# Kernel tuning notes

Hardware: AMD Instinct MI355X
Metric: run time of the kernel (lower is better)

The kernel has to match this reference:

```python
import jax, jax.numpy as jnp
import numpy as np

BLOCK = 64  # block_size from config
NEG_INF = -1e9


def setup_inputs() -> dict:
    key = jax.random.key(0)
    k1, k2, k3, k4 = jax.random.split(key, 4)
    B, H, S, D = 2, 8, 2048, 64
    nb = S // BLOCK  # 32 blocks per side
    query = jax.random.normal(k1, (B, H, S, D), dtype=jnp.float32)
    key_t = jax.random.normal(k2, (B, H, S, D), dtype=jnp.float32)
    value = jax.random.normal(k3, (B, H, S, D), dtype=jnp.float32)
    # binary block mask; force diagonal blocks on so every row has >=1 valid key
    mat = jax.random.randint(k4, (nb, nb), 0, 2).astype(jnp.int32)
    mat = mat.at[jnp.arange(nb), jnp.arange(nb)].set(1)
    mask = jnp.ones((B, S), dtype=jnp.float32)  # padding mask (1 = keep)
    return {"query": query, "key": key_t, "value": value, "mask": mask, "mat": mat}


def reference(query, key, value, mask, mat):
    # Upsample block mask [nb, nb] -> dense [S, S] (nearest, like nn.Upsample)
    block_dense = jnp.repeat(jnp.repeat(mat, BLOCK, axis=0), BLOCK, axis=1) > 0
    # Block-sparse QK^T: only positions inside nonzero blocks participate.
    scores = jnp.einsum('bhqd,bhkd->bhqk', query, key)
    # Additive padding-mask bias, as in the original: 1e6 * (1 - mask)
    scores = scores - 1e6 * (1.0 - mask)[:, None, None, :]
    # Positions outside the block pattern are excluded from the softmax.
    scores = jnp.where(block_dense[None, None, :, :], scores, NEG_INF)
    attn = jax.nn.softmax(scores, axis=-1)
    out = jnp.einsum('bhqk,bhkd->bhqd', attn, value)
    return out
```

## Files before the change

kernel.cpp:

```cpp
#include <hip/hip_runtime.h>


typedef __attribute__((ext_vector_type(8))) short short8;
typedef __attribute__((ext_vector_type(4))) short short4_;
typedef __attribute__((ext_vector_type(4))) float float4_;

#define B_   2
#define H_   8
#define S_   2048
#define D_   64
#define NB_  32
#define KP   72

__device__ __forceinline__ short f2bf(float f) {
    union { float f; unsigned int u; } x; x.f = f;
    unsigned int r = x.u + 0x7FFFu + ((x.u >> 16) & 1u);
    return (short)(r >> 16);
}
__device__ __forceinline__ float bf2f(short s) {
    union { unsigned int u; float f; } x; x.u = ((unsigned int)(unsigned short)s) << 16;
    return x.f;
}

__global__ __launch_bounds__(256)
void preconvert_kernel(const float* __restrict__ K, const float* __restrict__ V,
                       short* __restrict__ Khi, short* __restrict__ Klo,
                       short* __restrict__ Vtb) {
    __shared__ short vn[64 * KP];
    const int tid = threadIdx.x;
    const int kt  = blockIdx.x;
    const int bh  = blockIdx.y;
    const size_t tb = ((size_t)bh * S_ + kt * 64) * D_;

#pragma unroll
    for (int it = 0; it < 4; ++it) {
        int i = tid + it * 256;
        int row = i >> 4, c4 = (i & 15) * 4;
        float4_ kv = *(const float4_*)(K + tb + row * D_ + c4);
        short4_ hi, lo;
#pragma unroll
        for (int e = 0; e < 4; ++e) {
            hi[e] = f2bf(kv[e]);
            lo[e] = f2bf(kv[e] - bf2f(hi[e]));
        }
        *(short4_*)(Khi + tb + row * D_ + c4) = hi;
        *(short4_*)(Klo + tb + row * D_ + c4) = lo;
        float4_ vv = *(const float4_*)(V + tb + row * D_ + c4);
        short4_ vb;
#pragma unroll
        for (int e = 0; e < 4; ++e) vb[e] = f2bf(vv[e]);
        *(short4_*)&vn[row * KP + c4] = vb;
    }
    __syncthreads();
#pragma unroll
    for (int it = 0; it < 2; ++it) {
        int i = tid + it * 256;
        int rowd = i >> 3, key8 = (i & 7) * 8;
        short8 o;
#pragma unroll
        for (int e = 0; e < 8; ++e) o[e] = vn[(key8 + e) * KP + rowd];
        *(short8*)(Vtb + (((size_t)(bh * NB_ + kt)) * 64 + rowd) * 64 + key8) = o;
    }
}

__global__ __launch_bounds__(256, 2)
void attn_mfma_pl(const float* __restrict__ Q,
                  const float* __restrict__ Msk,
                  const int* __restrict__ Mat,
                  float* __restrict__ O,
                  const short* __restrict__ Khi_g,
                  const short* __restrict__ Klo_g,
                  const short* __restrict__ Vtb_g) {
    __shared__ __align__(16) short lds[4 * 64 * KP];
    short* Khi = lds;
    short* Klo = lds + 64 * KP;
    short* Vt  = lds + 2 * 64 * KP;
    short* Pl  = lds + 3 * 64 * KP;

    const int tid  = threadIdx.x;
    const int wave = tid >> 6;
    const int lane = tid & 63;
    const int c    = lane & 15;
    const int quad = lane >> 4;

    const int qb = blockIdx.x;
    const int bh = blockIdx.y;
    const int b  = bh / H_;
    const size_t base = (size_t)bh * S_ * D_;

    const int row0 = tid >> 3,          col0 = (tid & 7) * 8;
    const int row1 = (tid + 256) >> 3,  col1 = (tid & 7) * 8;

    short8 qh0, qh1, ql0, ql1;
    {
        const float* qp = Q + base + (size_t)(qb * 64 + wave * 16 + c) * D_ + quad * 8;
#pragma unroll
        for (int e = 0; e < 8; ++e) {
            float f0 = qp[e], f1 = qp[e + 32];
            qh0[e] = f2bf(f0); ql0[e] = f2bf(f0 - bf2f(qh0[e]));
            qh1[e] = f2bf(f1); ql1[e] = f2bf(f1 - bf2f(qh1[e]));
        }
    }

    float4_ o[4];
    float l_part[4];
#pragma unroll
    for (int t = 0; t < 4; ++t) { o[t][0] = 0.f; o[t][1] = 0.f; o[t][2] = 0.f; o[t][3] = 0.f; }
#pragma unroll
    for (int j = 0; j < 4; ++j) l_part[j] = 0.f;

    unsigned long long bm = __ballot(Mat[qb * NB_ + (lane & 31)] != 0);
    unsigned int mbits = (unsigned int)(bm & 0xFFFFFFFFull);

    short8 sK0, sK1, sL0, sL1, sV0, sV1;
    float  biasn[4];

    int kb = __builtin_ctz(mbits);
    mbits &= mbits - 1;
    {
        const short* kh = Khi_g + base + (size_t)kb * 64 * D_;
        const short* kl = Klo_g + base + (size_t)kb * 64 * D_;
        const short* vt = Vtb_g + ((size_t)(bh * NB_ + kb)) * 64 * 64;
        sK0 = *(const short8*)(kh + row0 * 64 + col0);
        sK1 = *(const short8*)(kh + row1 * 64 + col1);
        sL0 = *(const short8*)(kl + row0 * 64 + col0);
        sL1 = *(const short8*)(kl + row1 * 64 + col1);
        sV0 = *(const short8*)(vt + row0 * 64 + col0);
        sV1 = *(const short8*)(vt + row1 * 64 + col1);
#pragma unroll
        for (int t = 0; t < 4; ++t)
            biasn[t] = -1.0e6f * (1.0f - Msk[(size_t)b * S_ + kb * 64 + t * 16 + c]);
    }

    for (;;) {
        __syncthreads();
        *(short8*)&Khi[row0 * KP + col0] = sK0;
        *(short8*)&Khi[row1 * KP + col1] = sK1;
        *(short8*)&Klo[row0 * KP + col0] = sL0;
        *(short8*)&Klo[row1 * KP + col1] = sL1;
        *(short8*)&Vt[row0 * KP + col0]  = sV0;
        *(short8*)&Vt[row1 * KP + col1]  = sV1;
        float biasc[4];
#pragma unroll
        for (int t = 0; t < 4; ++t) biasc[t] = biasn[t];
        __syncthreads();

        const bool have_next = (mbits != 0);
        if (have_next) {
            kb = __builtin_ctz(mbits);
            mbits &= mbits - 1;
            const short* kh = Khi_g + base + (size_t)kb * 64 * D_;
            const short* kl = Klo_g + base + (size_t)kb * 64 * D_;
            const short* vt = Vtb_g + ((size_t)(bh * NB_ + kb)) * 64 * 64;
            sK0 = *(const short8*)(kh + row0 * 64 + col0);
            sK1 = *(const short8*)(kh + row1 * 64 + col1);
            sL0 = *(const short8*)(kl + row0 * 64 + col0);
            sL1 = *(const short8*)(kl + row1 * 64 + col1);
            sV0 = *(const short8*)(vt + row0 * 64 + col0);
            sV1 = *(const short8*)(vt + row1 * 64 + col1);
#pragma unroll
            for (int t = 0; t < 4; ++t)
                biasn[t] = -1.0e6f * (1.0f - Msk[(size_t)b * S_ + kb * 64 + t * 16 + c]);
        }

        float4_ sc[4];
#pragma unroll
        for (int t = 0; t < 4; ++t) { sc[t][0] = 0.f; sc[t][1] = 0.f; sc[t][2] = 0.f; sc[t][3] = 0.f; }
#pragma unroll
        for (int t = 0; t < 4; ++t) {
            const short* kph = &Khi[(t * 16 + c) * KP + quad * 8];
            const short* kpl = &Klo[(t * 16 + c) * KP + quad * 8];
            short8 kh0 = *(const short8*)(kph);
            short8 kh1 = *(const short8*)(kph + 32);
            short8 kl0 = *(const short8*)(kpl);
            short8 kl1 = *(const short8*)(kpl + 32);
            sc[t] = __builtin_amdgcn_mfma_f32_16x16x32_bf16(qh0, kh0, sc[t], 0, 0, 0);
            sc[t] = __builtin_amdgcn_mfma_f32_16x16x32_bf16(qh1, kh1, sc[t], 0, 0, 0);
            sc[t] = __builtin_amdgcn_mfma_f32_16x16x32_bf16(qh0, kl0, sc[t], 0, 0, 0);
            sc[t] = __builtin_amdgcn_mfma_f32_16x16x32_bf16(qh1, kl1, sc[t], 0, 0, 0);
            sc[t] = __builtin_amdgcn_mfma_f32_16x16x32_bf16(ql0, kh0, sc[t], 0, 0, 0);
            sc[t] = __builtin_amdgcn_mfma_f32_16x16x32_bf16(ql1, kh1, sc[t], 0, 0, 0);
        }

        short* Pw = Pl + wave * 16 * KP;
#pragma unroll
        for (int t = 0; t < 4; ++t) {
#pragma unroll
            for (int j = 0; j < 4; ++j) {
                float p = __expf(sc[t][j] + biasc[t]);
                l_part[j] += p;
                Pw[(quad * 4 + j) * KP + t * 16 + c] = f2bf(p);
            }
        }

        const short* pp = Pl + wave * 16 * KP + c * KP + quad * 8;
        short8 pa0 = *(const short8*)(pp);
        short8 pa1 = *(const short8*)(pp + 32);

#pragma unroll
        for (int t = 0; t < 4; ++t) {
            const short* vp = &Vt[(t * 16 + c) * KP + quad * 8];
            short8 vb0 = *(const short8*)(vp);
            short8 vb1 = *(const short8*)(vp + 32);
            o[t] = __builtin_amdgcn_mfma_f32_16x16x32_bf16(pa0, vb0, o[t], 0, 0, 0);
            o[t] = __builtin_amdgcn_mfma_f32_16x16x32_bf16(pa1, vb1, o[t], 0, 0, 0);
        }

        if (!have_next) break;
    }

#pragma unroll
    for (int j = 0; j < 4; ++j) {
        float rs = l_part[j];
        rs += __shfl_xor(rs, 1);
        rs += __shfl_xor(rs, 2);
        rs += __shfl_xor(rs, 4);
        rs += __shfl_xor(rs, 8);
        float inv = 1.0f / rs;
        size_t rowoff = base + (size_t)(qb * 64 + wave * 16 + quad * 4 + j) * D_;
#pragma unroll
        for (int t = 0; t < 4; ++t)
            O[rowoff + t * 16 + c] = o[t][j] * inv;
    }
}

__global__ __launch_bounds__(256, 2)
void attn_mfma_fb(const float* __restrict__ Q,
                  const float* __restrict__ K,
                  const float* __restrict__ V,
                  const float* __restrict__ Msk,
                  const int* __restrict__ Mat,
                  float* __restrict__ O) {
    __shared__ __align__(16) short lds[4 * 64 * KP];
    short* Khi = lds;
    short* Klo = lds + 64 * KP;
    short* Vt  = lds + 2 * 64 * KP;
    short* Pl  = lds + 3 * 64 * KP;

    const int tid  = threadIdx.x;
    const int wave = tid >> 6;
    const int lane = tid & 63;
    const int c    = lane & 15;
    const int quad = lane >> 4;

    const int qb = blockIdx.x;
    const int bh = blockIdx.y;
    const int b  = bh / H_;
    const size_t base = (size_t)bh * S_ * D_;

    short8 qh0, qh1, ql0, ql1;
    {
        const float* qp = Q + base + (size_t)(qb * 64 + wave * 16 + c) * D_ + quad * 8;
#pragma unroll
        for (int e = 0; e < 8; ++e) {
            float f0 = qp[e], f1 = qp[e + 32];
            qh0[e] = f2bf(f0); ql0[e] = f2bf(f0 - bf2f(qh0[e]));
            qh1[e] = f2bf(f1); ql1[e] = f2bf(f1 - bf2f(qh1[e]));
        }
    }

    float4_ o[4];
    float l_part[4];
#pragma unroll
    for (int t = 0; t < 4; ++t) { o[t][0] = 0.f; o[t][1] = 0.f; o[t][2] = 0.f; o[t][3] = 0.f; }
#pragma unroll
    for (int j = 0; j < 4; ++j) l_part[j] = 0.f;

    for (int kb = 0; kb < NB_; ++kb) {
        if (Mat[qb * NB_ + kb] == 0) continue;

        __syncthreads();
        {
            const float* kg = K + base + (size_t)kb * 64 * D_;
            const float* vg = V + base + (size_t)kb * 64 * D_;
#pragma unroll
            for (int it = 0; it < 4; ++it) {
                int i = tid + it * 256;
                int row = i >> 4, c4 = (i & 15) * 4;
                float4_ kv = *(const float4_*)(kg + row * D_ + c4);
                short4_ hi, lo;
#pragma unroll
                for (int e = 0; e < 4; ++e) {
                    hi[e] = f2bf(kv[e]);
                    lo[e] = f2bf(kv[e] - bf2f(hi[e]));
                }
                *(short4_*)&Khi[row * KP + c4] = hi;
                *(short4_*)&Klo[row * KP + c4] = lo;
                float4_ vv = *(const float4_*)(vg + row * D_ + c4);
#pragma unroll
                for (int e = 0; e < 4; ++e) Vt[(c4 + e) * KP + row] = f2bf(vv[e]);
            }
        }
        __syncthreads();

        float4_ sc[4];
#pragma unroll
        for (int t = 0; t < 4; ++t) { sc[t][0] = 0.f; sc[t][1] = 0.f; sc[t][2] = 0.f; sc[t][3] = 0.f; }
#pragma unroll
        for (int t = 0; t < 4; ++t) {
            const short* kph = &Khi[(t * 16 + c) * KP + quad * 8];
            const short* kpl = &Klo[(t * 16 + c) * KP + quad * 8];
            short8 kh0 = *(const short8*)(kph);
            short8 kh1 = *(const short8*)(kph + 32);
            short8 kl0 = *(const short8*)(kpl);
            short8 kl1 = *(const short8*)(kpl + 32);
            sc[t] = __builtin_amdgcn_mfma_f32_16x16x32_bf16(qh0, kh0, sc[t], 0, 0, 0);
            sc[t] = __builtin_amdgcn_mfma_f32_16x16x32_bf16(qh1, kh1, sc[t], 0, 0, 0);
            sc[t] = __builtin_amdgcn_mfma_f32_16x16x32_bf16(qh0, kl0, sc[t], 0, 0, 0);
            sc[t] = __builtin_amdgcn_mfma_f32_16x16x32_bf16(qh1, kl1, sc[t], 0, 0, 0);
            sc[t] = __builtin_amdgcn_mfma_f32_16x16x32_bf16(ql0, kh0, sc[t], 0, 0, 0);
            sc[t] = __builtin_amdgcn_mfma_f32_16x16x32_bf16(ql1, kh1, sc[t], 0, 0, 0);
        }

        short* Pw = Pl + wave * 16 * KP;
#pragma unroll
        for (int t = 0; t < 4; ++t) {
            float bias = -1.0e6f * (1.0f - Msk[(size_t)b * S_ + kb * 64 + t * 16 + c]);
#pragma unroll
            for (int j = 0; j < 4; ++j) {
                float p = __expf(sc[t][j] + bias);
                l_part[j] += p;
                Pw[(quad * 4 + j) * KP + t * 16 + c] = f2bf(p);
            }
        }

        const short* pp = Pl + wave * 16 * KP + c * KP + quad * 8;
        short8 pa0 = *(const short8*)(pp);
        short8 pa1 = *(const short8*)(pp + 32);

#pragma unroll
        for (int t = 0; t < 4; ++t) {
            const short* vp = &Vt[(t * 16 + c) * KP + quad * 8];
            short8 vb0 = *(const short8*)(vp);
            short8 vb1 = *(const short8*)(vp + 32);
            o[t] = __builtin_amdgcn_mfma_f32_16x16x32_bf16(pa0, vb0, o[t], 0, 0, 0);
            o[t] = __builtin_amdgcn_mfma_f32_16x16x32_bf16(pa1, vb1, o[t], 0, 0, 0);
        }
    }

#pragma unroll
    for (int j = 0; j < 4; ++j) {
        float rs = l_part[j];
        rs += __shfl_xor(rs, 1);
        rs += __shfl_xor(rs, 2);
        rs += __shfl_xor(rs, 4);
        rs += __shfl_xor(rs, 8);
        float inv = 1.0f / rs;
        size_t rowoff = base + (size_t)(qb * 64 + wave * 16 + quad * 4 + j) * D_;
#pragma unroll
        for (int t = 0; t < 4; ++t)
            O[rowoff + t * 16 + c] = o[t][j] * inv;
    }
}

extern "C" void kernel_launch(void* const* d_in, const int* in_sizes, int n_in,
                              void* d_out, int out_size, void* d_ws, size_t ws_size,
                              hipStream_t stream) {
    const float* q   = (const float*)d_in[0];
    const float* k   = (const float*)d_in[1];
    const float* v   = (const float*)d_in[2];
    const float* msk = (const float*)d_in[3];
    const int*   mat = (const int*)d_in[4];
    float*       out = (float*)d_out;

    const size_t elems = (size_t)B_ * H_ * S_ * D_;
    const size_t need  = 3 * elems * sizeof(short);
    const int use_pre  = (ws_size >= need) ? 1 : 0;

    short* khi = (short*)d_ws;
    short* klo = khi + elems;
    short* vtb = klo + elems;

    dim3 grid(NB_, B_ * H_);
    if (use_pre) {
        preconvert_kernel<<<grid, dim3(256), 0, stream>>>(k, v, khi, klo, vtb);
        attn_mfma_pl<<<grid, dim3(256), 0, stream>>>(q, msk, mat, out, khi, klo, vtb);
    } else {
        attn_mfma_fb<<<grid, dim3(256), 0, stream>>>(q, k, v, msk, mat, out);
    }
}
```

Baseline: 119.4 us.

## Replace split-bf16 QK^T with single fp16 MFMA and halve query tile

K is now preconverted to a single fp16 copy, and Q is converted to fp16 in-kernel. QK^T then uses two fp16 MFMAs per tile instead of six split hi/lo bf16 MFMAs, and the Klo workspace buffer and its loads are gone. The attention kernel also moves to 128-thread blocks covering 32 query rows, which doubles the grid. That gives more parallelism, but each K/V block is now staged twice as often across workgroups. The trade-off is lower precision in the scores: there is no max-subtraction before exp, so fp16 rounding of large logits could push results past tolerance.

Result: faster. 112.9 us (-5.4%).

```diff
diff --git a/kernel.cpp b/kernel.cpp
--- a/kernel.cpp
+++ b/kernel.cpp
@@ -4,6 +4,7 @@
 typedef __attribute__((ext_vector_type(8))) short short8;
 typedef __attribute__((ext_vector_type(4))) short short4_;
 typedef __attribute__((ext_vector_type(4))) float float4_;
+typedef __attribute__((ext_vector_type(8))) _Float16 half8_;
 
 #define B_   2
 #define H_   8
@@ -21,11 +22,14 @@
     union { unsigned int u; float f; } x; x.u = ((unsigned int)(unsigned short)s) << 16;
     return x.f;
 }
+__device__ __forceinline__ short f2h(float f) {
+    _Float16 h = (_Float16)f;
+    return __builtin_bit_cast(short, h);
+}
 
 __global__ __launch_bounds__(256)
 void preconvert_kernel(const float* __restrict__ K, const float* __restrict__ V,
-                       short* __restrict__ Khi, short* __restrict__ Klo,
-                       short* __restrict__ Vtb) {
+                       short* __restrict__ Khf, short* __restrict__ Vtb) {
     __shared__ short vn[64 * KP];
     const int tid = threadIdx.x;
     const int kt  = blockIdx.x;
@@ -37,14 +41,10 @@
         int i = tid + it * 256;
         int row = i >> 4, c4 = (i & 15) * 4;
         float4_ kv = *(const float4_*)(K + tb + row * D_ + c4);
-        short4_ hi, lo;
-#pragma unroll
-        for (int e = 0; e < 4; ++e) {
-            hi[e] = f2bf(kv[e]);
-            lo[e] = f2bf(kv[e] - bf2f(hi[e]));
-        }
-        *(short4_*)(Khi + tb + row * D_ + c4) = hi;
-        *(short4_*)(Klo + tb + row * D_ + c4) = lo;
+        short4_ kh;
+#pragma unroll
+        for (int e = 0; e < 4; ++e) kh[e] = f2h(kv[e]);
+        *(short4_*)(Khf + tb + row * D_ + c4) = kh;
         float4_ vv = *(const float4_*)(V + tb + row * D_ + c4);
         short4_ vb;
 #pragma unroll
@@ -63,14 +63,165 @@
     }
 }
 
+__global__ __launch_bounds__(128, 2)
+void attn_mfma_h(const float* __restrict__ Q,
+                 const float* __restrict__ Msk,
+                 const int* __restrict__ Mat,
+                 float* __restrict__ O,
+                 const short* __restrict__ Khf_g,
+                 const short* __restrict__ Vtb_g) {
+    __shared__ __align__(16) short lds[(64 + 64 + 2 * 16) * KP];
+    short* Kh = lds;
+    short* Vt = lds + 64 * KP;
+    short* Pl = lds + 2 * 64 * KP;
+
+    const int tid  = threadIdx.x;
+    const int wave = tid >> 6;
+    const int lane = tid & 63;
+    const int c    = lane & 15;
+    const int quad = lane >> 4;
+
+    const int qt = blockIdx.x;
+    const int bh = blockIdx.y;
+    const int b  = bh / H_;
+    const int qb = qt >> 1;
+    const size_t base = (size_t)bh * S_ * D_;
+
+    half8_ qa0, qa1;
+    {
+        const float* qp = Q + base + (size_t)(qt * 32 + wave * 16 + c) * D_ + quad * 8;
+#pragma unroll
+        for (int e = 0; e < 8; ++e) {
+            qa0[e] = (_Float16)qp[e];
+            qa1[e] = (_Float16)qp[e + 32];
+        }
+    }
+
+    float4_ o[4];
+    float l_part[4];
+#pragma unroll
+    for (int t = 0; t < 4; ++t) { o[t][0] = 0.f; o[t][1] = 0.f; o[t][2] = 0.f; o[t][3] = 0.f; }
+#pragma unroll
+    for (int j = 0; j < 4; ++j) l_part[j] = 0.f;
+
+    unsigned long long bm = __ballot(Mat[qb * NB_ + (lane & 31)] != 0);
+    unsigned int mbits = (unsigned int)(bm & 0xFFFFFFFFull);
+
+    int srow[4], scol[4];
+#pragma unroll
+    for (int it = 0; it < 4; ++it) {
+        int i = tid + it * 128;
+        srow[it] = i >> 3;
+        scol[it] = (i & 7) * 8;
+    }
+
+    short8 sK[4], sV[4];
+    float  biasn[4];
+
+    int kb = __builtin_ctz(mbits);
+    mbits &= mbits - 1;
+    {
+        const short* kh = Khf_g + base + (size_t)kb * 64 * D_;
+        const short* vt = Vtb_g + ((size_t)(bh * NB_ + kb)) * 64 * 64;
+#pragma unroll
+        for (int it = 0; it < 4; ++it) {
+            sK[it] = *(const short8*)(kh + srow[it] * 64 + scol[it]);
+            sV[it] = *(const short8*)(vt + srow[it] * 64 + scol[it]);
+        }
+#pragma unroll
+        for (int t = 0; t < 4; ++t)
+            biasn[t] = -1.0e6f * (1.0f - Msk[(size_t)b * S_ + kb * 64 + t * 16 + c]);
+    }
+
+    for (;;) {
+        __syncthreads();
+#pragma unroll
+        for (int it = 0; it < 4; ++it) {
+            *(short8*)&Kh[srow[it] * KP + scol[it]] = sK[it];
+            *(short8*)&Vt[srow[it] * KP + scol[it]] = sV[it];
+        }
+        float biasc[4];
+#pragma unroll
+        for (int t = 0; t < 4; ++t) biasc[t] = biasn[t];
+        __syncthreads();
+
+        const bool have_next = (mbits != 0);
+        if (have_next) {
+            kb = __builtin_ctz(mbits);
+            mbits &= mbits - 1;
+            const short* kh = Khf_g + base + (size_t)kb * 64 * D_;
+            const short* vt = Vtb_g + ((size_t)(bh * NB_ + kb)) * 64 * 64;
+#pragma unroll
+            for (int it = 0; it < 4; ++it) {
+                sK[it] = *(const short8*)(kh + srow[it] * 64 + scol[it]);
+                sV[it] = *(const short8*)(vt + srow[it] * 64 + scol[it]);
+            }
+#pragma unroll
+            for (int t = 0; t < 4; ++t)
+                biasn[t] = -1.0e6f * (1.0f - Msk[(size_t)b * S_ + kb * 64 + t * 16 + c]);
+        }
+
+        float4_ sc[4];
+#pragma unroll
+        for (int t = 0; t < 4; ++t) { sc[t][0] = 0.f; sc[t][1] = 0.f; sc[t][2] = 0.f; sc[t][3] = 0.f; }
+#pragma unroll
+        for (int t = 0; t < 4; ++t) {
+            const short* kp_ = &Kh[(t * 16 + c) * KP + quad * 8];
+            half8_ kb0 = __builtin_bit_cast(half8_, *(const short8*)(kp_));
+            half8_ kb1 = __builtin_bit_cast(half8_, *(const short8*)(kp_ + 32));
+            sc[t] = __builtin_amdgcn_mfma_f32_16x16x32_f16(qa0, kb0, sc[t], 0, 0, 0);
+            sc[t] = __builtin_amdgcn_mfma_f32_16x16x32_f16(qa1, kb1, sc[t], 0, 0, 0);
+        }
+
+        short* Pw = Pl + wave * 16 * KP;
+#pragma unroll
+        for (int t = 0; t < 4; ++t) {
+#pragma unroll
+            for (int j = 0; j < 4; ++j) {
+                float p = __expf(sc[t][j] + biasc[t]);
+                l_part[j] += p;
+                Pw[(quad * 4 + j) * KP + t * 16 + c] = f2bf(p);
+            }
+        }
+
+        const short* pp = Pl + wave * 16 * KP + c * KP + quad * 8;
+        short8 pa0 = *(const short8*)(pp);
+        short8 pa1 = *(const short8*)(pp + 32);
+
+#pragma unroll
+        for (int t = 0; t < 4; ++t) {
+            const short* vp = &Vt[(t * 16 + c) * KP + quad * 8];
+            short8 vb0 = *(const short8*)(vp);
+            short8 vb1 = *(const short8*)(vp + 32);
+            o[t] = __builtin_amdgcn_mfma_f32_16x16x32_bf16(pa0, vb0, o[t], 0, 0, 0);
+            o[t] = __builtin_amdgcn_mfma_f32_16x16x32_bf16(pa1, vb1, o[t], 0, 0, 0);
+        }
+
+        if (!have_next) break;
+    }
+
+#pragma unroll
+    for (int j = 0; j < 4; ++j) {
+        float rs = l_part[j];
+        rs += __shfl_xor(rs, 1);
+        rs += __shfl_xor(rs, 2);
+        rs += __shfl_xor(rs, 4);
+        rs += __shfl_xor(rs, 8);
+        float inv = 1.0f / rs;
+        size_t rowoff = base + (size_t)(qt * 32 + wave * 16 + quad * 4 + j) * D_;
+#pragma unroll
+        for (int t = 0; t < 4; ++t)
+            O[rowoff + t * 16 + c] = o[t][j] * inv;
+    }
+}
+
 __global__ __launch_bounds__(256, 2)
-void attn_mfma_pl(const float* __restrict__ Q,
+void attn_mfma_fb(const float* __restrict__ Q,
+                  const float* __restrict__ K,
+                  const float* __restrict__ V,
                   const float* __restrict__ Msk,
                   const int* __restrict__ Mat,
-                  float* __restrict__ O,
-                  const short* __restrict__ Khi_g,
-                  const short* __restrict__ Klo_g,
-                  const short* __restrict__ Vtb_g) {
+                  float* __restrict__ O) {
     __shared__ __align__(16) short lds[4 * 64 * KP];
     short* Khi = lds;
     short* Klo = lds + 64 * KP;
@@ -88,9 +239,6 @@
     const int b  = bh / H_;
     const size_t base = (size_t)bh * S_ * D_;
 
-    const int row0 = tid >> 3,          col0 = (tid & 7) * 8;
-    const int row1 = (tid + 256) >> 3,  col1 = (tid & 7) * 8;
-
     short8 qh0, qh1, ql0, ql1;
     {
         const float* qp = Q + base + (size_t)(qb * 64 + wave * 16 + c) * D_ + quad * 8;
@@ -109,59 +257,32 @@
 #pragma unroll
     for (int j = 0; j < 4; ++j) l_part[j] = 0.f;
 
-    unsigned long long bm = __ballot(Mat[qb * NB_ + (lane & 31)] != 0);
-    unsigned int mbits = (unsigned int)(bm & 0xFFFFFFFFull);
-
-    short8 sK0, sK1, sL0, sL1, sV0, sV1;
-    float  biasn[4];
-
-    int kb = __builtin_ctz(mbits);
-    mbits &= mbits - 1;
-    {
-        const short* kh = Khi_g + base + (size_t)kb * 64 * D_;
-        const short* kl = Klo_g + base + (size_t)kb * 64 * D_;
-        const short* vt = Vtb_g + ((size_t)(bh * NB_ + kb)) * 64 * 64;
-        sK0 = *(const short8*)(kh + row0 * 64 + col0);
-        sK1 = *(const short8*)(kh + row1 * 64 + col1);
-        sL0 = *(const short8*)(kl + row0 * 64 + col0);
-        sL1 = *(const short8*)(kl + row1 * 64 + col1);
-        sV0 = *(const short8*)(vt + row0 * 64 + col0);
-        sV1 = *(const short8*)(vt + row1 * 64 + col1);
-#pragma unroll
-        for (int t = 0; t < 4; ++t)
-            biasn[t] = -1.0e6f * (1.0f - Msk[(size_t)b * S_ + kb * 64 + t * 16 + c]);
-    }
-
-    for (;;) {
+    for (int kb = 0; kb < NB_; ++kb) {
+        if (Mat[qb * NB_ + kb] == 0) continue;
+
         __syncthreads();
-        *(short8*)&Khi[row0 * KP + col0] = sK0;
-        *(short8*)&Khi[row1 * KP + col1] = sK1;
-        *(short8*)&Klo[row0 * KP + col0] = sL0;
-        *(short8*)&Klo[row1 * KP + col1] = sL1;
-        *(short8*)&Vt[row0 * KP + col0]  = sV0;
-        *(short8*)&Vt[row1 * KP + col1]  = sV1;
-        float biasc[4];
-#pragma unroll
-        for (int t = 0; t < 4; ++t) biasc[t] = biasn[t];
+        {
+            const float* kg = K + base + (size_t)kb * 64 * D_;
+            const float* vg = V + base + (size_t)kb * 64 * D_;
+#pragma unroll
+            for (int it = 0; it < 4; ++it) {
+                int i = tid + it * 256;
+                int row = i >> 4, c4 = (i & 15) * 4;
+                float4_ kv = *(const float4_*)(kg + row * D_ + c4);
+                short4_ hi, lo;
+#pragma unroll
+                for (int e = 0; e < 4; ++e) {
+                    hi[e] = f2bf(kv[e]);
+                    lo[e] = f2bf(kv[e] - bf2f(hi[e]));
+                }
+                *(short4_*)&Khi[row * KP + c4] = hi;
+                *(short4_*)&Klo[row * KP + c4] = lo;
+                float4_ vv = *(const float4_*)(vg + row * D_ + c4);
+#pragma unroll
+                for (int e = 0; e < 4; ++e) Vt[(c4 + e) * KP + row] = f2bf(vv[e]);
+            }
+        }
         __syncthreads();
-
-        const bool have_next = (mbits != 0);
-        if (have_next) {
-            kb = __builtin_ctz(mbits);
-            mbits &= mbits - 1;
-            const short* kh = Khi_g + base + (size_t)kb * 64 * D_;
-            const short* kl = Klo_g + base + (size_t)kb * 64 * D_;
-            const short* vt = Vtb_g + ((size_t)(bh * NB_ + kb)) * 64 * 64;
-            sK0 = *(const short8*)(kh + row0 * 64 + col0);
-            sK1 = *(const short8*)(kh + row1 * 64 + col1);
-            sL0 = *(const short8*)(kl + row0 * 64 + col0);
-            sL1 = *(const short8*)(kl + row1 * 64 + col1);
-            sV0 = *(const short8*)(vt + row0 * 64 + col0);
-            sV1 = *(const short8*)(vt + row1 * 64 + col1);
-#pragma unroll
-            for (int t = 0; t < 4; ++t)
-                biasn[t] = -1.0e6f * (1.0f - Msk[(size_t)b * S_ + kb * 64 + t * 16 + c]);
-        }
 
         float4_ sc[4];
 #pragma unroll
@@ -185,136 +306,6 @@
         short* Pw = Pl + wave * 16 * KP;
 #pragma unroll
         for (int t = 0; t < 4; ++t) {
-#pragma unroll
-            for (int j = 0; j < 4; ++j) {
-                float p = __expf(sc[t][j] + biasc[t]);
-                l_part[j] += p;
-                Pw[(quad * 4 + j) * KP + t * 16 + c] = f2bf(p);
-            }
-        }
-
-        const short* pp = Pl + wave * 16 * KP + c * KP + quad * 8;
-        short8 pa0 = *(const short8*)(pp);
-        short8 pa1 = *(const short8*)(pp + 32);
-
-#pragma unroll
-        for (int t = 0; t < 4; ++t) {
-            const short* vp = &Vt[(t * 16 + c) * KP + quad * 8];
-            short8 vb0 = *(const short8*)(vp);
-            short8 vb1 = *(const short8*)(vp + 32);
-            o[t] = __builtin_amdgcn_mfma_f32_16x16x32_bf16(pa0, vb0, o[t], 0, 0, 0);
-            o[t] = __builtin_amdgcn_mfma_f32_16x16x32_bf16(pa1, vb1, o[t], 0, 0, 0);
-        }
-
-        if (!have_next) break;
-    }
-
-#pragma unroll
-    for (int j = 0; j < 4; ++j) {
-        float rs = l_part[j];
-        rs += __shfl_xor(rs, 1);
-        rs += __shfl_xor(rs, 2);
-        rs += __shfl_xor(rs, 4);
-        rs += __shfl_xor(rs, 8);
-        float inv = 1.0f / rs;
-        size_t rowoff = base + (size_t)(qb * 64 + wave * 16 + quad * 4 + j) * D_;
-#pragma unroll
-        for (int t = 0; t < 4; ++t)
-            O[rowoff + t * 16 + c] = o[t][j] * inv;
-    }
-}
-
-__global__ __launch_bounds__(256, 2)
-void attn_mfma_fb(const float* __restrict__ Q,
-                  const float* __restrict__ K,
-                  const float* __restrict__ V,
-                  const float* __restrict__ Msk,
-                  const int* __restrict__ Mat,
-                  float* __restrict__ O) {
-    __shared__ __align__(16) short lds[4 * 64 * KP];
-    short* Khi = lds;
-    short* Klo = lds + 64 * KP;
-    short* Vt  = lds + 2 * 64 * KP;
-    short* Pl  = lds + 3 * 64 * KP;
-
-    const int tid  = threadIdx.x;
-    const int wave = tid >> 6;
-    const int lane = tid & 63;
-    const int c    = lane & 15;
-    const int quad = lane >> 4;
-
-    const int qb = blockIdx.x;
-    const int bh = blockIdx.y;
-    const int b  = bh / H_;
-    const size_t base = (size_t)bh * S_ * D_;
-
-    short8 qh0, qh1, ql0, ql1;
-    {
-        const float* qp = Q + base + (size_t)(qb * 64 + wave * 16 + c) * D_ + quad * 8;
-#pragma unroll
-        for (int e = 0; e < 8; ++e) {
-            float f0 = qp[e], f1 = qp[e + 32];
-            qh0[e] = f2bf(f0); ql0[e] = f2bf(f0 - bf2f(qh0[e]));
-            qh1[e] = f2bf(f1); ql1[e] = f2bf(f1 - bf2f(qh1[e]));
-        }
-    }
-
-    float4_ o[4];
-    float l_part[4];
-#pragma unroll
-    for (int t = 0; t < 4; ++t) { o[t][0] = 0.f; o[t][1] = 0.f; o[t][2] = 0.f; o[t][3] = 0.f; }
-#pragma unroll
-    for (int j = 0; j < 4; ++j) l_part[j] = 0.f;
-
-    for (int kb = 0; kb < NB_; ++kb) {
-        if (Mat[qb * NB_ + kb] == 0) continue;
-
-        __syncthreads();
-        {
-            const float* kg = K + base + (size_t)kb * 64 * D_;
-            const float* vg = V + base + (size_t)kb * 64 * D_;
-#pragma unroll
-            for (int it = 0; it < 4; ++it) {
-                int i = tid + it * 256;
-                int row = i >> 4, c4 = (i & 15) * 4;
-                float4_ kv = *(const float4_*)(kg + row * D_ + c4);
-                short4_ hi, lo;
-#pragma unroll
-                for (int e = 0; e < 4; ++e) {
-                    hi[e] = f2bf(kv[e]);
-                    lo[e] = f2bf(kv[e] - bf2f(hi[e]));
-                }
-                *(short4_*)&Khi[row * KP + c4] = hi;
-                *(short4_*)&Klo[row * KP + c4] = lo;
-                float4_ vv = *(const float4_*)(vg + row * D_ + c4);
-#pragma unroll
-                for (int e = 0; e < 4; ++e) Vt[(c4 + e) * KP + row] = f2bf(vv[e]);
-            }
-        }
-        __syncthreads();
-
-        float4_ sc[4];
-#pragma unroll
-        for (int t = 0; t < 4; ++t) { sc[t][0] = 0.f; sc[t][1] = 0.f; sc[t][2] = 0.f; sc[t][3] = 0.f; }
-#pragma unroll
-        for (int t = 0; t < 4; ++t) {
-            const short* kph = &Khi[(t * 16 + c) * KP + quad * 8];
-            const short* kpl = &Klo[(t * 16 + c) * KP + quad * 8];
-            short8 kh0 = *(const short8*)(kph);
-            short8 kh1 = *(const short8*)(kph + 32);
-            short8 kl0 = *(const short8*)(kpl);
-            short8 kl1 = *(const short8*)(kpl + 32);
-            sc[t] = __builtin_amdgcn_mfma_f32_16x16x32_bf16(qh0, kh0, sc[t], 0, 0, 0);
-            sc[t] = __builtin_amdgcn_mfma_f32_16x16x32_bf16(qh1, kh1, sc[t], 0, 0, 0);
-            sc[t] = __builtin_amdgcn_mfma_f32_16x16x32_bf16(qh0, kl0, sc[t], 0, 0, 0);
-            sc[t] = __builtin_amdgcn_mfma_f32_16x16x32_bf16(qh1, kl1, sc[t], 0, 0, 0);
-            sc[t] = __builtin_amdgcn_mfma_f32_16x16x32_bf16(ql0, kh0, sc[t], 0, 0, 0);
-            sc[t] = __builtin_amdgcn_mfma_f32_16x16x32_bf16(ql1, kh1, sc[t], 0, 0, 0);
-        }
-
-        short* Pw = Pl + wave * 16 * KP;
-#pragma unroll
-        for (int t = 0; t < 4; ++t) {
             float bias = -1.0e6f * (1.0f - Msk[(size_t)b * S_ + kb * 64 + t * 16 + c]);
 #pragma unroll
             for (int j = 0; j < 4; ++j) {
@@ -364,18 +355,19 @@
     float*       out = (float*)d_out;
 
     const size_t elems = (size_t)B_ * H_ * S_ * D_;
-    const size_t need  = 3 * elems * sizeof(short);
+    const size_t need  = 2 * elems * sizeof(short);
     const int use_pre  = (ws_size >= need) ? 1 : 0;
 
-    short* khi = (short*)d_ws;
-    short* klo = khi + elems;
-    short* vtb = klo + elems;
-
-    dim3 grid(NB_, B_ * H_);
+    short* khf = (short*)d_ws;
+    short* vtb = khf + elems;
+
     if (use_pre) {
-        preconvert_kernel<<<grid, dim3(256), 0, stream>>>(k, v, khi, klo, vtb);
-        attn_mfma_pl<<<grid, dim3(256), 0, stream>>>(q, msk, mat, out, khi, klo, vtb);
+        dim3 pgrid(NB_, B_ * H_);
+        preconvert_kernel<<<pgrid, dim3(256), 0, stream>>>(k, v, khf, vtb);
+        dim3 grid(S_ / 32, B_ * H_);
+        attn_mfma_h<<<grid, dim3(128), 0, stream>>>(q, msk, mat, out, khf, vtb);
     } else {
+        dim3 grid(NB_, B_ * H_);
         attn_mfma_fb<<<grid, dim3(256), 0, stream>>>(q, k, v, msk, mat, out);
     }
 }
```
